# Optimization experiments

Measured on AMD Instinct MI355X. Metric: run time of the kernel, lower is better.

The kernel has to match this reference:

```python
import jax, jax.numpy as jnp
import numpy as np

NUM_USERS = 100000
NUM_ITEMS = 50000
N_NODES = NUM_USERS + NUM_ITEMS
N_EDGES = 3200000
EMB_DIM = 128
N_LAYERS = 3


def setup_inputs() -> dict:
    key = jax.random.key(0)
    ks = jax.random.split(key, 7)
    # nn.init.normal_(std=0.1) embedding init
    user_emb = jax.random.normal(ks[0], (NUM_USERS, EMB_DIM), dtype=jnp.float32) * 0.1
    item_emb = jax.random.normal(ks[1], (NUM_ITEMS, EMB_DIM), dtype=jnp.float32) * 0.1
    # static normalized adjacency in COO form (values from D^-1/2 A D^-1/2 are positive)
    edge_row = jax.random.randint(ks[2], (N_EDGES,), 0, N_NODES, dtype=jnp.int32)
    edge_col = jax.random.randint(ks[3], (N_EDGES,), 0, N_NODES, dtype=jnp.int32)
    edge_val = jax.random.uniform(ks[4], (N_EDGES,), dtype=jnp.float32)
    users = jax.random.randint(ks[5], (2048,), 0, NUM_USERS, dtype=jnp.int32)
    items = jax.random.randint(ks[6], (2048,), 0, NUM_ITEMS, dtype=jnp.int32)
    return {
        "user_emb": user_emb,
        "item_emb": item_emb,
        "edge_val": edge_val,
        "edge_row": edge_row,
        "edge_col": edge_col,
        "users": users,
        "items": items,
    }


def reference(user_emb, item_emb, edge_val, edge_row, edge_col, users, items):
    # computer(): concat user/item tables -> [N, d]
    all_emb = jnp.concatenate([user_emb, item_emb], axis=0)
    acc = all_emb  # running sum of layer embeddings (fused mean over layers)
    emb = all_emb
    for _ in range(N_LAYERS):
        # sparse.mm(G, emb): per-edge gather, scale, scatter-add
        msg = edge_val[:, None] * emb[edge_col]  # [E, d]
        emb = jax.ops.segment_sum(msg, edge_row, num_segments=N_NODES)
        acc = acc + emb
    light_out = acc / jnp.float32(N_LAYERS + 1)  # mean over stacked layer embeddings
    users_emb = light_out[users]
    items_emb = light_out[NUM_USERS + items]
    # gamma = sum(users_emb * items_emb, dim=1)
    return jnp.sum(users_emb * items_emb, axis=1)
```

## Files before the change

kernel.cpp:

```cpp
#include <hip/hip_runtime.h>

#define D 128
#define NUSERS 100000
#define NITEMS 50000
#define NNODES 150000
#define NEDGES 3200000
#define NSEL 2048
#define NBKT 586
#define PBLK 256
#define EPB (NEDGES / PBLK)
#define MATN (NBKT * PBLK)
#define MB ((MATN + 255) / 256)
#define BCAP 8192
#define INIT_BLKS 2048
#define SEL_BLKS ((2 * NSEL * D) / 256)
#define FLG_BLKS ((NNODES + 255) / 256)
#define COLMASK 0x3FFFFu

typedef unsigned int uint_t;
typedef unsigned short ushort_t;

__device__ inline uint_t bf16_rne(float f) {
    uint_t x = __float_as_uint(f);
    return (x + 0x7FFFu + ((x >> 16) & 1u)) >> 16;
}

__device__ inline int block_excl_scan(int v, int* lds, int nw) {
    int lane = threadIdx.x & 63;
    int wid = (int)(threadIdx.x >> 6);
    int x = v;
    #pragma unroll
    for (int off = 1; off < 64; off <<= 1) {
        int y = __shfl_up(x, off);
        if (lane >= off) x += y;
    }
    if (lane == 63) lds[wid] = x;
    __syncthreads();
    if (wid == 0) {
        int s = (lane < nw) ? lds[lane] : 0;
        #pragma unroll
        for (int off = 1; off < 16; off <<= 1) {
            int y = __shfl_up(s, off);
            if (lane >= off) s += y;
        }
        if (lane < nw) lds[lane] = s;
    }
    __syncthreads();
    int waveoff = (wid == 0) ? 0 : lds[wid - 1];
    return waveoff + x - v;
}

__global__ void k_prologue(const int* __restrict__ row, int* __restrict__ mat,
                           const float4* __restrict__ u4, const float4* __restrict__ i4,
                           uint4* __restrict__ cur,
                           const float* __restrict__ user_emb,
                           const float* __restrict__ item_emb,
                           const int* __restrict__ users, const int* __restrict__ items,
                           float* __restrict__ acc, int* __restrict__ flags) {
    __shared__ int h[NBKT];
    int blk = blockIdx.x;
    if (blk < PBLK) {
        for (int i = threadIdx.x; i < NBKT; i += 256) h[i] = 0;
        __syncthreads();
        int beg = blk * EPB, end = beg + EPB;
        for (int e = beg + threadIdx.x; e < end; e += 256)
            atomicAdd(&h[row[e] >> 8], 1);
        __syncthreads();
        for (int i = threadIdx.x; i < NBKT; i += 256)
            mat[i * PBLK + blk] = h[i];
    } else if (blk < PBLK + INIT_BLKS) {
        size_t total8 = (size_t)NNODES * D / 8;
        size_t ub8 = (size_t)NUSERS * D / 8;
        size_t stride = (size_t)INIT_BLKS * 256;
        for (size_t i = (size_t)(blk - PBLK) * 256 + threadIdx.x; i < total8; i += stride) {
            const float4* src = (i < ub8) ? &u4[2 * i] : &i4[2 * (i - ub8)];
            float4 a = src[0], b = src[1];
            uint4 o;
            o.x = (bf16_rne(a.y) << 16) | bf16_rne(a.x);
            o.y = (bf16_rne(a.w) << 16) | bf16_rne(a.z);
            o.z = (bf16_rne(b.y) << 16) | bf16_rne(b.x);
            o.w = (bf16_rne(b.w) << 16) | bf16_rne(b.z);
            cur[i] = o;
        }
    } else if (blk < PBLK + INIT_BLKS + SEL_BLKS) {
        int idx = (blk - PBLK - INIT_BLKS) * 256 + threadIdx.x;
        if (idx < 2 * NSEL * D) {
            int r = idx >> 7;
            int d = idx & (D - 1);
            const float* src = (r < NSEL) ? &user_emb[(size_t)users[r] * D]
                                          : &item_emb[(size_t)items[r - NSEL] * D];
            acc[idx] = src[d];
        }
    } else {
        int i = (blk - PBLK - INIT_BLKS - SEL_BLKS) * 256 + threadIdx.x;
        if (i < NNODES) flags[i] = 0;
    }
}

__global__ void k_blocksum(const int* __restrict__ src, int* __restrict__ bsums, int n) {
    int i = blockIdx.x * 256 + threadIdx.x;
    int v = (i < n) ? src[i] : 0;
    #pragma unroll
    for (int off = 32; off; off >>= 1) v += __shfl_down(v, off);
    __shared__ int lds[4];
    int lane = threadIdx.x & 63, wid = (int)(threadIdx.x >> 6);
    if (lane == 0) lds[wid] = v;
    __syncthreads();
    if (threadIdx.x == 0) bsums[blockIdx.x] = lds[0] + lds[1] + lds[2] + lds[3];
}

__global__ void k_scan2(int* __restrict__ mat, const int* __restrict__ bsums, int n) {
    __shared__ int red[4];
    __shared__ int lds[4];
    int b = blockIdx.x;
    int lane = threadIdx.x & 63, wid = (int)(threadIdx.x >> 6);
    int s = 0;
    for (int j = threadIdx.x; j < b; j += 256) s += bsums[j];
    #pragma unroll
    for (int off = 32; off; off >>= 1) s += __shfl_down(s, off);
    if (lane == 0) red[wid] = s;
    __syncthreads();
    int base = red[0] + red[1] + red[2] + red[3];
    int i = b * 256 + threadIdx.x;
    int v = (i < n) ? mat[i] : 0;
    int ex = block_excl_scan(v, lds, 4);
    if (i < n) mat[i] = base + ex;
}

__global__ void k_p2(const int* __restrict__ row, const int* __restrict__ col,
                     const float* __restrict__ val, const int* __restrict__ mat,
                     int2* __restrict__ tmp) {
    __shared__ int cur[NBKT];
    for (int i = threadIdx.x; i < NBKT; i += 256)
        cur[i] = mat[i * PBLK + blockIdx.x];
    __syncthreads();
    int beg = blockIdx.x * EPB, end = beg + EPB;
    for (int e = beg + threadIdx.x; e < end; e += 256) {
        int r = row[e];
        int b = r >> 8;
        int pos = atomicAdd(&cur[b], 1);
        int q = (int)(val[e] * 16384.f + 0.5f);
        if (q > 16383) q = 16383;
        int2 rc;
        rc.x = r & 255;
        rc.y = (int)(((uint_t)q << 18) | (uint_t)col[e]);
        tmp[pos] = rc;
    }
}

__global__ void k_p3(const int2* __restrict__ tmp, const int* __restrict__ mat,
                     uint_t* __restrict__ recs, int* __restrict__ row_start) {
    __shared__ int2 buf[BCAP];
    __shared__ int h[256];
    __shared__ int lds[4];
    int b = blockIdx.x;
    int beg = mat[b * PBLK];
    int end = (b + 1 < NBKT) ? mat[(b + 1) * PBLK] : NEDGES;
    int n = end - beg;
    h[threadIdx.x] = 0;
    if (n <= BCAP) {
        for (int i = threadIdx.x; i < n; i += 256) buf[i] = tmp[beg + i];
        __syncthreads();
        for (int i = threadIdx.x; i < n; i += 256)
            atomicAdd(&h[buf[i].x], 1);
        __syncthreads();
        int ex = block_excl_scan(h[threadIdx.x], lds, 4);
        int rowid = b * 256 + threadIdx.x;
        if (rowid < NNODES) row_start[rowid] = beg + ex;
        if (b == NBKT - 1 && threadIdx.x == 0) row_start[NNODES] = NEDGES;
        h[threadIdx.x] = ex;
        __syncthreads();
        for (int i = threadIdx.x; i < n; i += 256) {
            int2 rc = buf[i];
            int pos = beg + atomicAdd(&h[rc.x], 1);
            recs[pos] = (uint_t)rc.y;
        }
    } else {
        __syncthreads();
        for (int e = beg + threadIdx.x; e < end; e += 256)
            atomicAdd(&h[tmp[e].x], 1);
        __syncthreads();
        int ex = block_excl_scan(h[threadIdx.x], lds, 4);
        int rowid = b * 256 + threadIdx.x;
        if (rowid < NNODES) row_start[rowid] = beg + ex;
        if (b == NBKT - 1 && threadIdx.x == 0) row_start[NNODES] = NEDGES;
        h[threadIdx.x] = ex;
        __syncthreads();
        for (int e = beg + threadIdx.x; e < end; e += 256) {
            int2 rc = tmp[e];
            int pos = beg + atomicAdd(&h[rc.x], 1);
            recs[pos] = (uint_t)rc.y;
        }
    }
}

__global__ void k_mark(const int* __restrict__ users, const int* __restrict__ items,
                       const int* __restrict__ row_start, const uint_t* __restrict__ recs,
                       int* __restrict__ flags) {
    int lane = threadIdx.x & 63;
    int w = (int)((blockIdx.x * blockDim.x + threadIdx.x) >> 6);
    if (w >= 2 * NSEL) return;
    int node = (w < NSEL) ? users[w] : NUSERS + items[w - NSEL];
    int beg = __builtin_amdgcn_readfirstlane(row_start[node]);
    int end = __builtin_amdgcn_readfirstlane(row_start[node + 1]);
    if (lane == 0) flags[node] = 1;
    for (int e = beg + lane; e < end; e += 64)
        flags[recs[e] & COLMASK] = 1;
}

__global__ void k_spmm_csr(const uint_t* __restrict__ emb, uint_t* __restrict__ outp,
                           const int* __restrict__ row_start,
                           const uint_t* __restrict__ recs,
                           const int* __restrict__ flags, int use_flags) {
    int lane = threadIdx.x & 63;
    int w = (int)((blockIdx.x * blockDim.x + threadIdx.x) >> 6);
    if (w >= NNODES) return;
    if (use_flags && __builtin_amdgcn_readfirstlane(flags[w]) == 0) return;
    int beg = __builtin_amdgcn_readfirstlane(row_start[w]);
    int end = __builtin_amdgcn_readfirstlane(row_start[w + 1]);
    float ax = 0.f, ay = 0.f;
    int e = beg;
    for (; e + 3 < end; e += 4) {
        uint_t q0 = recs[e], q1 = recs[e + 1], q2 = recs[e + 2], q3 = recs[e + 3];
        uint_t g0 = emb[(size_t)(q0 & COLMASK) * 64 + lane];
        uint_t g1 = emb[(size_t)(q1 & COLMASK) * 64 + lane];
        uint_t g2 = emb[(size_t)(q2 & COLMASK) * 64 + lane];
        uint_t g3 = emb[(size_t)(q3 & COLMASK) * 64 + lane];
        float v0 = (float)(q0 >> 18) * (1.f / 16384.f);
        float v1 = (float)(q1 >> 18) * (1.f / 16384.f);
        float v2 = (float)(q2 >> 18) * (1.f / 16384.f);
        float v3 = (float)(q3 >> 18) * (1.f / 16384.f);
        ax += v0 * __uint_as_float(g0 << 16) + v1 * __uint_as_float(g1 << 16)
            + v2 * __uint_as_float(g2 << 16) + v3 * __uint_as_float(g3 << 16);
        ay += v0 * __uint_as_float(g0 & 0xFFFF0000u) + v1 * __uint_as_float(g1 & 0xFFFF0000u)
            + v2 * __uint_as_float(g2 & 0xFFFF0000u) + v3 * __uint_as_float(g3 & 0xFFFF0000u);
    }
    for (; e < end; ++e) {
        uint_t q = recs[e];
        float v = (float)(q >> 18) * (1.f / 16384.f);
        uint_t g = emb[(size_t)(q & COLMASK) * 64 + lane];
        ax += v * __uint_as_float(g << 16);
        ay += v * __uint_as_float(g & 0xFFFF0000u);
    }
    outp[(size_t)w * 64 + lane] = (bf16_rne(ay) << 16) | bf16_rne(ax);
}

__global__ void k_spmm_sel(const uint_t* __restrict__ emb,
                           const int* __restrict__ users, const int* __restrict__ items,
                           const int* __restrict__ row_start,
                           const uint_t* __restrict__ recs,
                           float* __restrict__ acc) {
    int lane = threadIdx.x & 63;
    int w = (int)((blockIdx.x * blockDim.x + threadIdx.x) >> 6);
    if (w >= 2 * NSEL) return;
    int node = (w < NSEL) ? users[w] : NUSERS + items[w - NSEL];
    int beg = __builtin_amdgcn_readfirstlane(row_start[node]);
    int end = __builtin_amdgcn_readfirstlane(row_start[node + 1]);
    uint_t e2 = emb[(size_t)node * 64 + lane];
    float ax = __uint_as_float(e2 << 16);
    float ay = __uint_as_float(e2 & 0xFFFF0000u);
    for (int e = beg; e < end; ++e) {
        uint_t q = recs[e];
        float v = (float)(q >> 18) * (1.f / 16384.f);
        uint_t g = emb[(size_t)(q & COLMASK) * 64 + lane];
        ax += v * __uint_as_float(g << 16);
        ay += v * __uint_as_float(g & 0xFFFF0000u);
    }
    float2* p = (float2*)&acc[(size_t)w * D + lane * 2];
    float2 r = *p;
    r.x += ax; r.y += ay;
    *p = r;
}

__global__ void k_sel_bf16(const ushort_t* __restrict__ src,
                           const int* __restrict__ users, const int* __restrict__ items,
                           float* __restrict__ acc) {
    int idx = blockIdx.x * blockDim.x + threadIdx.x;
    if (idx >= 2 * NSEL * D) return;
    int r = idx >> 7;
    int d = idx & (D - 1);
    size_t node = (r < NSEL) ? (size_t)users[r] : (size_t)NUSERS + (size_t)items[r - NSEL];
    uint_t u = (uint_t)src[node * D + d] << 16;
    acc[idx] += __uint_as_float(u);
}

__global__ void k_dot(const float* __restrict__ acc, float* __restrict__ out) {
    int lane = threadIdx.x & 63;
    int w = (int)((blockIdx.x * blockDim.x + threadIdx.x) >> 6);
    if (w >= NSEL) return;
    const float* u = &acc[(size_t)w * D];
    const float* it = &acc[(size_t)(NSEL + w) * D];
    float s = u[lane] * it[lane] + u[lane + 64] * it[lane + 64];
    #pragma unroll
    for (int off = 32; off; off >>= 1) s += __shfl_down(s, off);
    if (lane == 0) out[w] = s * (1.0f / 16.0f);
}

extern "C" void kernel_launch(void* const* d_in, const int* in_sizes, int n_in,
                              void* d_out, int out_size, void* d_ws, size_t ws_size,
                              hipStream_t stream) {
    const float* user_emb = (const float*)d_in[0];
    const float* item_emb = (const float*)d_in[1];
    const float* edge_val = (const float*)d_in[2];
    const int*   edge_row = (const int*)d_in[3];
    const int*   edge_col = (const int*)d_in[4];
    const int*   users    = (const int*)d_in[5];
    const int*   items    = (const int*)d_in[6];
    float* out = (float*)d_out;

    const size_t tab = (size_t)NNODES * D;
    ushort_t* bufA   = (ushort_t*)d_ws;
    ushort_t* bufB   = bufA + tab;
    float* accs      = (float*)(bufB + tab);
    uint_t* recs     = (uint_t*)(accs + (size_t)2 * NSEL * D);
    int2*  tmp       = (int2*)(recs + NEDGES);
    int*   mat       = (int*)(tmp + NEDGES);
    int*   row_start = mat + MATN;
    int*   flags     = row_start + NNODES + 1;
    int*   bsums     = flags + NNODES;

    k_prologue<<<PBLK + INIT_BLKS + SEL_BLKS + FLG_BLKS, 256, 0, stream>>>(
        edge_row, mat, (const float4*)user_emb, (const float4*)item_emb,
        (uint4*)bufA, user_emb, item_emb, users, items, accs, flags);

    k_blocksum<<<MB, 256, 0, stream>>>(mat, bsums, MATN);
    k_scan2<<<MB, 256, 0, stream>>>(mat, bsums, MATN);
    k_p2<<<PBLK, 256, 0, stream>>>(edge_row, edge_col, edge_val, mat, tmp);
    k_p3<<<NBKT, 256, 0, stream>>>(tmp, mat, recs, row_start);
    k_mark<<<(2 * NSEL) / 4, 256, 0, stream>>>(users, items, row_start, recs, flags);

    k_spmm_csr<<<(NNODES + 3) / 4, 256, 0, stream>>>((const uint_t*)bufA, (uint_t*)bufB,
                                                     row_start, recs, flags, 0);
    k_sel_bf16<<<SEL_BLKS, 256, 0, stream>>>(bufB, users, items, accs);
    k_spmm_csr<<<(NNODES + 3) / 4, 256, 0, stream>>>((const uint_t*)bufB, (uint_t*)bufA,
                                                     row_start, recs, flags, 1);
    k_spmm_sel<<<(2 * NSEL) / 4, 256, 0, stream>>>((const uint_t*)bufA, users, items,
                                                   row_start, recs, accs);

    k_dot<<<512, 256, 0, stream>>>(accs, out);
}
```

Before: 329.9 us.

## Fuse selection marking into bucket sort and merge final layer with dot product

Marks selected rows in the scan kernel and sets neighbour flags during the bucket-sort scatter, which removes the separate k_mark pass. The temporary edge buffer is split into a 4-byte packed row/col word plus a 2-byte quantized value, shrinking it from 8 to 6 bytes per edge. The final selected-row SpMM, the bf16 accumulation, the layer-0 gather and the dot product are fused into one kernel, which removes the fp32 acc buffer and three launches. The cost is extra global flag writes inside k_p3 and an LDS exchange inside the final kernel.

```diff
diff --git a/kernel.cpp b/kernel.cpp
--- a/kernel.cpp
+++ b/kernel.cpp
@@ -13,8 +13,8 @@
 #define MB ((MATN + 255) / 256)
 #define BCAP 8192
 #define INIT_BLKS 2048
-#define SEL_BLKS ((2 * NSEL * D) / 256)
 #define FLG_BLKS ((NNODES + 255) / 256)
+#define SELSET_BLKS ((2 * NSEL + 255) / 256)
 #define COLMASK 0x3FFFFu
 
 typedef unsigned int uint_t;
@@ -53,10 +53,7 @@
 __global__ void k_prologue(const int* __restrict__ row, int* __restrict__ mat,
                            const float4* __restrict__ u4, const float4* __restrict__ i4,
                            uint4* __restrict__ cur,
-                           const float* __restrict__ user_emb,
-                           const float* __restrict__ item_emb,
-                           const int* __restrict__ users, const int* __restrict__ items,
-                           float* __restrict__ acc, int* __restrict__ flags) {
+                           int* __restrict__ flags, int* __restrict__ selflag) {
     __shared__ int h[NBKT];
     int blk = blockIdx.x;
     if (blk < PBLK) {
@@ -82,18 +79,9 @@
             o.w = (bf16_rne(b.w) << 16) | bf16_rne(b.z);
             cur[i] = o;
         }
-    } else if (blk < PBLK + INIT_BLKS + SEL_BLKS) {
-        int idx = (blk - PBLK - INIT_BLKS) * 256 + threadIdx.x;
-        if (idx < 2 * NSEL * D) {
-            int r = idx >> 7;
-            int d = idx & (D - 1);
-            const float* src = (r < NSEL) ? &user_emb[(size_t)users[r] * D]
-                                          : &item_emb[(size_t)items[r - NSEL] * D];
-            acc[idx] = src[d];
-        }
     } else {
-        int i = (blk - PBLK - INIT_BLKS - SEL_BLKS) * 256 + threadIdx.x;
-        if (i < NNODES) flags[i] = 0;
+        int i = (blk - PBLK - INIT_BLKS) * 256 + threadIdx.x;
+        if (i < NNODES) { flags[i] = 0; selflag[i] = 0; }
     }
 }
 
@@ -109,10 +97,21 @@
     if (threadIdx.x == 0) bsums[blockIdx.x] = lds[0] + lds[1] + lds[2] + lds[3];
 }
 
-__global__ void k_scan2(int* __restrict__ mat, const int* __restrict__ bsums, int n) {
+__global__ void k_scan2(int* __restrict__ mat, const int* __restrict__ bsums, int n,
+                        const int* __restrict__ users, const int* __restrict__ items,
+                        int* __restrict__ selflag, int* __restrict__ flags) {
+    int b = blockIdx.x;
+    if (b >= MB) {
+        int idx = (b - MB) * 256 + threadIdx.x;
+        if (idx < 2 * NSEL) {
+            int node = (idx < NSEL) ? users[idx] : NUSERS + items[idx - NSEL];
+            selflag[node] = 1;
+            flags[node] = 1;
+        }
+        return;
+    }
     __shared__ int red[4];
     __shared__ int lds[4];
-    int b = blockIdx.x;
     int lane = threadIdx.x & 63, wid = (int)(threadIdx.x >> 6);
     int s = 0;
     for (int j = threadIdx.x; j < b; j += 256) s += bsums[j];
@@ -129,7 +128,7 @@
 
 __global__ void k_p2(const int* __restrict__ row, const int* __restrict__ col,
                      const float* __restrict__ val, const int* __restrict__ mat,
-                     int2* __restrict__ tmp) {
+                     uint_t* __restrict__ t4, ushort_t* __restrict__ tv) {
     __shared__ int cur[NBKT];
     for (int i = threadIdx.x; i < NBKT; i += 256)
         cur[i] = mat[i * PBLK + blockIdx.x];
@@ -141,71 +140,65 @@
         int pos = atomicAdd(&cur[b], 1);
         int q = (int)(val[e] * 16384.f + 0.5f);
         if (q > 16383) q = 16383;
-        int2 rc;
-        rc.x = r & 255;
-        rc.y = (int)(((uint_t)q << 18) | (uint_t)col[e]);
-        tmp[pos] = rc;
-    }
-}
-
-__global__ void k_p3(const int2* __restrict__ tmp, const int* __restrict__ mat,
-                     uint_t* __restrict__ recs, int* __restrict__ row_start) {
-    __shared__ int2 buf[BCAP];
+        t4[pos] = ((uint_t)(r & 255) << 18) | (uint_t)col[e];
+        tv[pos] = (ushort_t)q;
+    }
+}
+
+__global__ void k_p3(const uint_t* __restrict__ t4, const ushort_t* __restrict__ tv,
+                     const int* __restrict__ mat, uint_t* __restrict__ recs,
+                     int* __restrict__ row_start,
+                     const int* __restrict__ selflag, int* __restrict__ flags) {
+    __shared__ uint_t b4[BCAP];
+    __shared__ ushort_t bv[BCAP];
     __shared__ int h[256];
     __shared__ int lds[4];
+    __shared__ unsigned char selb[256];
     int b = blockIdx.x;
     int beg = mat[b * PBLK];
     int end = (b + 1 < NBKT) ? mat[(b + 1) * PBLK] : NEDGES;
     int n = end - beg;
+    int rowid = b * 256 + threadIdx.x;
     h[threadIdx.x] = 0;
+    selb[threadIdx.x] = (rowid < NNODES) ? (unsigned char)selflag[rowid] : 0;
     if (n <= BCAP) {
-        for (int i = threadIdx.x; i < n; i += 256) buf[i] = tmp[beg + i];
+        for (int i = threadIdx.x; i < n; i += 256) { b4[i] = t4[beg + i]; bv[i] = tv[beg + i]; }
         __syncthreads();
         for (int i = threadIdx.x; i < n; i += 256)
-            atomicAdd(&h[buf[i].x], 1);
+            atomicAdd(&h[b4[i] >> 18], 1);
         __syncthreads();
         int ex = block_excl_scan(h[threadIdx.x], lds, 4);
-        int rowid = b * 256 + threadIdx.x;
         if (rowid < NNODES) row_start[rowid] = beg + ex;
         if (b == NBKT - 1 && threadIdx.x == 0) row_start[NNODES] = NEDGES;
         h[threadIdx.x] = ex;
         __syncthreads();
         for (int i = threadIdx.x; i < n; i += 256) {
-            int2 rc = buf[i];
-            int pos = beg + atomicAdd(&h[rc.x], 1);
-            recs[pos] = (uint_t)rc.y;
+            uint_t a = b4[i];
+            int r = (int)(a >> 18);
+            uint_t c = a & COLMASK;
+            int pos = beg + atomicAdd(&h[r], 1);
+            recs[pos] = ((uint_t)bv[i] << 18) | c;
+            if (selb[r]) flags[c] = 1;
         }
     } else {
         __syncthreads();
         for (int e = beg + threadIdx.x; e < end; e += 256)
-            atomicAdd(&h[tmp[e].x], 1);
+            atomicAdd(&h[t4[e] >> 18], 1);
         __syncthreads();
         int ex = block_excl_scan(h[threadIdx.x], lds, 4);
-        int rowid = b * 256 + threadIdx.x;
         if (rowid < NNODES) row_start[rowid] = beg + ex;
         if (b == NBKT - 1 && threadIdx.x == 0) row_start[NNODES] = NEDGES;
         h[threadIdx.x] = ex;
         __syncthreads();
         for (int e = beg + threadIdx.x; e < end; e += 256) {
-            int2 rc = tmp[e];
-            int pos = beg + atomicAdd(&h[rc.x], 1);
-            recs[pos] = (uint_t)rc.y;
-        }
-    }
-}
-
-__global__ void k_mark(const int* __restrict__ users, const int* __restrict__ items,
-                       const int* __restrict__ row_start, const uint_t* __restrict__ recs,
-                       int* __restrict__ flags) {
-    int lane = threadIdx.x & 63;
-    int w = (int)((blockIdx.x * blockDim.x + threadIdx.x) >> 6);
-    if (w >= 2 * NSEL) return;
-    int node = (w < NSEL) ? users[w] : NUSERS + items[w - NSEL];
-    int beg = __builtin_amdgcn_readfirstlane(row_start[node]);
-    int end = __builtin_amdgcn_readfirstlane(row_start[node + 1]);
-    if (lane == 0) flags[node] = 1;
-    for (int e = beg + lane; e < end; e += 64)
-        flags[recs[e] & COLMASK] = 1;
+            uint_t a = t4[e];
+            int r = (int)(a >> 18);
+            uint_t c = a & COLMASK;
+            int pos = beg + atomicAdd(&h[r], 1);
+            recs[pos] = ((uint_t)tv[e] << 18) | c;
+            if (selb[r]) flags[c] = 1;
+        }
+    }
 }
 
 __global__ void k_spmm_csr(const uint_t* __restrict__ emb, uint_t* __restrict__ outp,
@@ -245,55 +238,51 @@
     outp[(size_t)w * 64 + lane] = (bf16_rne(ay) << 16) | bf16_rne(ax);
 }
 
-__global__ void k_spmm_sel(const uint_t* __restrict__ emb,
-                           const int* __restrict__ users, const int* __restrict__ items,
-                           const int* __restrict__ row_start,
-                           const uint_t* __restrict__ recs,
-                           float* __restrict__ acc) {
+__global__ void k_final(const uint_t* __restrict__ embA,
+                        const uint_t* __restrict__ embB,
+                        const float* __restrict__ user_emb,
+                        const float* __restrict__ item_emb,
+                        const int* __restrict__ users, const int* __restrict__ items,
+                        const int* __restrict__ row_start, const uint_t* __restrict__ recs,
+                        float* __restrict__ out) {
+    __shared__ float ush[2][64][2];
     int lane = threadIdx.x & 63;
-    int w = (int)((blockIdx.x * blockDim.x + threadIdx.x) >> 6);
-    if (w >= 2 * NSEL) return;
-    int node = (w < NSEL) ? users[w] : NUSERS + items[w - NSEL];
+    int wid = (int)(threadIdx.x >> 6);
+    int pairIdx = blockIdx.x * 2 + (wid & 1);
+    int isItem = wid >> 1;
+    int node, idx0;
+    const float* e0p;
+    if (isItem) {
+        idx0 = items[pairIdx];
+        node = NUSERS + idx0;
+        e0p = &item_emb[(size_t)idx0 * D];
+    } else {
+        idx0 = users[pairIdx];
+        node = idx0;
+        e0p = &user_emb[(size_t)idx0 * D];
+    }
+    const float2 e0 = *(const float2*)(&e0p[lane * 2]);
+    uint_t u1 = embB[(size_t)node * 64 + lane];
+    uint_t u2 = embA[(size_t)node * 64 + lane];
+    float ax = e0.x + __uint_as_float(u1 << 16) + __uint_as_float(u2 << 16);
+    float ay = e0.y + __uint_as_float(u1 & 0xFFFF0000u) + __uint_as_float(u2 & 0xFFFF0000u);
     int beg = __builtin_amdgcn_readfirstlane(row_start[node]);
     int end = __builtin_amdgcn_readfirstlane(row_start[node + 1]);
-    uint_t e2 = emb[(size_t)node * 64 + lane];
-    float ax = __uint_as_float(e2 << 16);
-    float ay = __uint_as_float(e2 & 0xFFFF0000u);
     for (int e = beg; e < end; ++e) {
         uint_t q = recs[e];
         float v = (float)(q >> 18) * (1.f / 16384.f);
-        uint_t g = emb[(size_t)(q & COLMASK) * 64 + lane];
+        uint_t g = embA[(size_t)(q & COLMASK) * 64 + lane];
         ax += v * __uint_as_float(g << 16);
         ay += v * __uint_as_float(g & 0xFFFF0000u);
     }
-    float2* p = (float2*)&acc[(size_t)w * D + lane * 2];
-    float2 r = *p;
-    r.x += ax; r.y += ay;
-    *p = r;
-}
-
-__global__ void k_sel_bf16(const ushort_t* __restrict__ src,
-                           const int* __restrict__ users, const int* __restrict__ items,
-                           float* __restrict__ acc) {
-    int idx = blockIdx.x * blockDim.x + threadIdx.x;
-    if (idx >= 2 * NSEL * D) return;
-    int r = idx >> 7;
-    int d = idx & (D - 1);
-    size_t node = (r < NSEL) ? (size_t)users[r] : (size_t)NUSERS + (size_t)items[r - NSEL];
-    uint_t u = (uint_t)src[node * D + d] << 16;
-    acc[idx] += __uint_as_float(u);
-}
-
-__global__ void k_dot(const float* __restrict__ acc, float* __restrict__ out) {
-    int lane = threadIdx.x & 63;
-    int w = (int)((blockIdx.x * blockDim.x + threadIdx.x) >> 6);
-    if (w >= NSEL) return;
-    const float* u = &acc[(size_t)w * D];
-    const float* it = &acc[(size_t)(NSEL + w) * D];
-    float s = u[lane] * it[lane] + u[lane + 64] * it[lane + 64];
-    #pragma unroll
-    for (int off = 32; off; off >>= 1) s += __shfl_down(s, off);
-    if (lane == 0) out[w] = s * (1.0f / 16.0f);
+    if (!isItem) { ush[wid][lane][0] = ax; ush[wid][lane][1] = ay; }
+    __syncthreads();
+    if (isItem) {
+        float s = ush[wid - 2][lane][0] * ax + ush[wid - 2][lane][1] * ay;
+        #pragma unroll
+        for (int off = 32; off; off >>= 1) s += __shfl_down(s, off);
+        if (lane == 0) out[pairIdx] = s * (1.0f / 16.0f);
+    }
 }
 
 extern "C" void kernel_launch(void* const* d_in, const int* in_sizes, int n_in,
@@ -311,31 +300,30 @@
     const size_t tab = (size_t)NNODES * D;
     ushort_t* bufA   = (ushort_t*)d_ws;
     ushort_t* bufB   = bufA + tab;
-    float* accs      = (float*)(bufB + tab);
-    uint_t* recs     = (uint_t*)(accs + (size_t)2 * NSEL * D);
-    int2*  tmp       = (int2*)(recs + NEDGES);
-    int*   mat       = (int*)(tmp + NEDGES);
+    uint_t* recs     = (uint_t*)(bufB + tab);
+    uint_t* t4       = recs + NEDGES;
+    ushort_t* tv     = (ushort_t*)(t4 + NEDGES);
+    int*   mat       = (int*)(tv + NEDGES);
     int*   row_start = mat + MATN;
     int*   flags     = row_start + NNODES + 1;
-    int*   bsums     = flags + NNODES;
-
-    k_prologue<<<PBLK + INIT_BLKS + SEL_BLKS + FLG_BLKS, 256, 0, stream>>>(
+    int*   selflag   = flags + NNODES;
+    int*   bsums     = selflag + NNODES;
+
+    k_prologue<<<PBLK + INIT_BLKS + FLG_BLKS, 256, 0, stream>>>(
         edge_row, mat, (const float4*)user_emb, (const float4*)item_emb,
-        (uint4*)bufA, user_emb, item_emb, users, items, accs, flags);
+        (uint4*)bufA, flags, selflag);
 
     k_blocksum<<<MB, 256, 0, stream>>>(mat, bsums, MATN);
-    k_scan2<<<MB, 256, 0, stream>>>(mat, bsums, MATN);
-    k_p2<<<PBLK, 256, 0, stream>>>(edge_row, edge_col, edge_val, mat, tmp);
-    k_p3<<<NBKT, 256, 0, stream>>>(tmp, mat, recs, row_start);
-    k_mark<<<(2 * NSEL) / 4, 256, 0, stream>>>(users, items, row_start, recs, flags);
+    k_scan2<<<MB + SELSET_BLKS, 256, 0, stream>>>(mat, bsums, MATN,
+                                                  users, items, selflag, flags);
+    k_p2<<<PBLK, 256, 0, stream>>>(edge_row, edge_col, edge_val, mat, t4, tv);
+    k_p3<<<NBKT, 256, 0, stream>>>(t4, tv, mat, recs, row_start, selflag, flags);
 
     k_spmm_csr<<<(NNODES + 3) / 4, 256, 0, stream>>>((const uint_t*)bufA, (uint_t*)bufB,
                                                      row_start, recs, flags, 0);
-    k_sel_bf16<<<SEL_BLKS, 256, 0, stream>>>(bufB, users, items, accs);
     k_spmm_csr<<<(NNODES + 3) / 4, 256, 0, stream>>>((const uint_t*)bufB, (uint_t*)bufA,
                                                      row_start, recs, flags, 1);
-    k_spmm_sel<<<(2 * NSEL) / 4, 256, 0, stream>>>((const uint_t*)bufA, users, items,
-                                                   row_start, recs, accs);
-
-    k_dot<<<512, 256, 0, stream>>>(accs, out);
-}
+    k_final<<<NSEL / 2, 256, 0, stream>>>((const uint_t*)bufA, (const uint_t*)bufB,
+                                          user_emb, item_emb, users, items,
+                                          row_start, recs, out);
+}
```

New measurement: 334.2 us. Within noise of the previous version (+1.3%).
